# Kernel optimization log

Hardware: AMD Instinct MI355X
Metric: run time of the kernel (lower is better)

Reference implementation:

```python
import jax, jax.numpy as jnp
import numpy as np

N, E, IN_C, HID, OUT_C, HEADS, NUM_CLASSES = 50000, 800000, 128, 64, 64, 4, 40
NEG_SLOPE = 0.2


def _gat_conv(x, src, dst, W, a_src, a_dst, bias, heads, concat):
    # x: [N, F_in]; W: [F_in, heads*C]; a_src/a_dst: [1, heads, C]; bias: [out]
    n = x.shape[0]
    h = (x @ W).reshape(n, heads, -1)                      # [N, H, C]
    alpha_s = (h * a_src).sum(-1)                          # [N, H]
    alpha_d = (h * a_dst).sum(-1)                          # [N, H]
    e = jax.nn.leaky_relu(alpha_s[src] + alpha_d[dst], NEG_SLOPE)  # [E, H]
    # scatter-softmax over incoming edges of each dst node
    emax = jax.ops.segment_max(e, dst, num_segments=n)
    emax = jnp.where(jnp.isfinite(emax), emax, 0.0)
    ee = jnp.exp(e - emax[dst])
    denom = jax.ops.segment_sum(ee, dst, num_segments=n) + 1e-16
    w = ee / denom[dst]                                    # [E, H]
    out = jax.ops.segment_sum(h[src] * w[:, :, None], dst, num_segments=n)  # [N, H, C]
    out = out.reshape(n, -1) if concat else out.mean(axis=1)
    return out + bias


def setup_inputs() -> dict:
    key = jax.random.key(0)
    ks = jax.random.split(key, 12)
    s1 = 1.0 / np.sqrt(IN_C)
    s2 = 1.0 / np.sqrt(HID * HEADS)
    s3 = 1.0 / np.sqrt(OUT_C)
    return {
        "x": jax.random.normal(ks[0], (N, IN_C), dtype=jnp.float32),
        "edge_index": jax.random.randint(ks[1], (2, E), 0, N, dtype=jnp.int64),
        "W1": jax.random.normal(ks[2], (IN_C, HEADS * HID), dtype=jnp.float32) * s1,
        "att_src1": jax.random.normal(ks[3], (1, HEADS, HID), dtype=jnp.float32) * s1,
        "att_dst1": jax.random.normal(ks[4], (1, HEADS, HID), dtype=jnp.float32) * s1,
        "b1": jnp.zeros((HEADS * HID,), dtype=jnp.float32),
        "W2": jax.random.normal(ks[5], (HEADS * HID, OUT_C), dtype=jnp.float32) * s2,
        "att_src2": jax.random.normal(ks[6], (1, 1, OUT_C), dtype=jnp.float32) * s2,
        "att_dst2": jax.random.normal(ks[7], (1, 1, OUT_C), dtype=jnp.float32) * s2,
        "b2": jnp.zeros((OUT_C,), dtype=jnp.float32),
        "fc_w": jax.random.normal(ks[8], (OUT_C, NUM_CLASSES), dtype=jnp.float32) * s3,
        "fc_b": jnp.zeros((NUM_CLASSES,), dtype=jnp.float32),
    }


def reference(x, edge_index, W1, att_src1, att_dst1, b1, W2, att_src2, att_dst2, b2, fc_w, fc_b):
    n = x.shape[0]
    loops = jnp.arange(n, dtype=edge_index.dtype)
    ei = jnp.concatenate([edge_index, jnp.stack([loops, loops])], axis=1)  # add self-loops (PyG default)
    src, dst = ei[0], ei[1]
    h = jax.nn.relu(_gat_conv(x, src, dst, W1, att_src1, att_dst1, b1, HEADS, True))
    h = jax.nn.relu(_gat_conv(h, src, dst, W2, att_src2, att_dst2, b2, 1, False))
    # dropout p=0.01 is identity in eval mode
    pooled = h.mean(axis=0, keepdims=True)                 # global mean pool -> [1, OUT_C]
    logits = pooled @ fc_w + fc_b
    return jax.nn.log_softmax(logits, axis=1)
```

## Files before the change

### kernel.cpp

```cpp
#include <hip/hip_runtime.h>
#include <hip/hip_bf16.h>
#include <math.h>

#define NEG_SLOPE 0.2f
#define CHUNK2 2048
#define PGROUPS 32

typedef __attribute__((ext_vector_type(8))) short bf16x8;
typedef __attribute__((ext_vector_type(4))) float f32x4;
typedef __attribute__((ext_vector_type(2))) float f32x2_t;

__device__ __forceinline__ float lrelu(float a) { return a >= 0.f ? a : NEG_SLOPE * a; }
__device__ __forceinline__ unsigned short f2bu(float v) {
  unsigned u = __float_as_uint(v);
  u += 0x7fffu + ((u >> 16) & 1u);
  return (unsigned short)(u >> 16);
}
__device__ __forceinline__ unsigned char f2fp8(float v) {
  return (unsigned char)(__builtin_amdgcn_cvt_pk_fp8_f32(v, v, 0, false) & 0xFF);
}
__device__ __forceinline__ void fp8x4_dec(unsigned v, float& a, float& b, float& c, float& d) {
  f32x2_t lo = __builtin_amdgcn_cvt_pk_f32_fp8(v, false);
  f32x2_t hi = __builtin_amdgcn_cvt_pk_f32_fp8(v, true);
  a = lo.x; b = lo.y; c = hi.x; d = hi.y;
}

__global__ __launch_bounds__(256) void prep_kernel(
    const float* __restrict__ W1, unsigned short* __restrict__ w1t,
    const float* __restrict__ W2, unsigned short* __restrict__ w2t,
    const int* __restrict__ ei, int* __restrict__ bhist, int* __restrict__ done,
    int* __restrict__ bucketOff, int* __restrict__ cursor, int* __restrict__ rowptrN,
    float* __restrict__ pooled_grp,
    int E0, int Etot, int NBUCK, int wBlocks, int histBlocks) {
  __shared__ int hsm[256];
  __shared__ int rank;
  int t = threadIdx.x;
  if (blockIdx.x < (unsigned)wBlocks) {
    const int tot1 = 128 * 256, tot2 = 256 * 64;
    for (int i = blockIdx.x * 256 + t; i < tot1 + tot2; i += wBlocks * 256) {
      if (i < tot1) { int k = i >> 8, n = i & 255; w1t[n * 128 + k] = f2bu(W1[i]); }
      else { int j = i - tot1; int k = j >> 6, n = j & 63; w2t[n * 256 + k] = f2bu(W2[j]); }
    }
  } else {
    int bid = blockIdx.x - wBlocks;
    hsm[t] = 0;
    __syncthreads();
    for (int e = bid * 256 + t; e < Etot; e += histBlocks * 256) {
      int dst = (e < E0) ? ei[E0 + e] : (e - E0);
      atomicAdd(&hsm[dst >> 8], 1);
    }
    __syncthreads();
    if (t < NBUCK && hsm[t]) atomicAdd(&bhist[t], hsm[t]);
    __threadfence();
    if (t == 0) rank = atomicAdd(done, 1);
    __syncthreads();
    if (rank == histBlocks - 1) {
      int v = (t < NBUCK) ? atomicAdd(&bhist[t], 0) : 0;
      __syncthreads();
      hsm[t] = v;
      __syncthreads();
      for (int off = 1; off < 256; off <<= 1) {
        int u = (t >= off) ? hsm[t - off] : 0;
        __syncthreads();
        hsm[t] += u;
        __syncthreads();
      }
      int excl = hsm[t] - v;
      if (t < NBUCK) { bucketOff[t] = excl; cursor[t] = excl; }
      if (t == 0) { bucketOff[NBUCK] = Etot; *rowptrN = Etot; }
      for (int i = t; i < PGROUPS * 64; i += 256) pooled_grp[i] = 0.f;
    }
  }
}

__device__ void gemm1_tile(const float* __restrict__ x,
    const unsigned short* __restrict__ BT, unsigned char* __restrict__ C8,
    const float* __restrict__ att_s, const float* __restrict__ att_d,
    float* __restrict__ as_, float* __restrict__ ad_,
    int M, int bx, int by, char* smem) {
  const int K = 128;
  unsigned short (*Al)[40] = (unsigned short (*)[40])smem;
  unsigned short (*Bt)[40] = (unsigned short (*)[40])(smem + 5120);
  float* sal = (float*)(smem + 10240);
  float* sad = (float*)(smem + 10752);
  const int tid = threadIdx.x;
  const int row0 = by * 64, col0 = bx * 64;
  const int lane = tid & 63, wave = tid >> 6;
  const int wm = wave >> 1, wn = wave & 1;
  const int l15 = lane & 15, q = lane >> 4;

  f32x4 acc[2][2] = {};

  const int rr = tid >> 2, rc = (tid & 3) * 8;

  for (int k0 = 0; k0 < K; k0 += 32) {
    float4 v0 = make_float4(0.f, 0.f, 0.f, 0.f), v1 = v0;
    if (row0 + rr < M) {
      const float* ap = x + (size_t)(row0 + rr) * K + k0 + rc;
      v0 = *(const float4*)ap;
      v1 = *(const float4*)(ap + 4);
    }
    *(ushort4*)&Al[rr][rc] = make_ushort4(f2bu(v0.x), f2bu(v0.y), f2bu(v0.z), f2bu(v0.w));
    *(ushort4*)&Al[rr][rc + 4] = make_ushort4(f2bu(v1.x), f2bu(v1.y), f2bu(v1.z), f2bu(v1.w));
    {
      const ushort4* bp = (const ushort4*)(BT + (size_t)(col0 + rr) * K + k0 + rc);
      *(ushort4*)&Bt[rr][rc] = bp[0];
      *(ushort4*)&Bt[rr][rc + 4] = bp[1];
    }
    __syncthreads();
    bf16x8 af[2], bf[2];
#pragma unroll
    for (int mi = 0; mi < 2; mi++)
      af[mi] = *(const bf16x8*)&Al[wm * 32 + mi * 16 + l15][q * 8];
#pragma unroll
    for (int ni = 0; ni < 2; ni++)
      bf[ni] = *(const bf16x8*)&Bt[wn * 32 + ni * 16 + l15][q * 8];
#pragma unroll
    for (int mi = 0; mi < 2; mi++)
#pragma unroll
      for (int ni = 0; ni < 2; ni++)
        acc[mi][ni] = __builtin_amdgcn_mfma_f32_16x16x32_bf16(af[mi], bf[ni], acc[mi][ni], 0, 0, 0);
    __syncthreads();
  }
#pragma unroll
  for (int mi = 0; mi < 2; mi++) {
#pragma unroll
    for (int r = 0; r < 4; r++) {
      int grow = row0 + wm * 32 + mi * 16 + q * 4 + r;
      if (grow < M) {
#pragma unroll
        for (int ni = 0; ni < 2; ni++) {
          int gcol = col0 + wn * 32 + ni * 16 + l15;
          C8[(size_t)grow * 256 + gcol] = f2fp8(acc[mi][ni][r]);
        }
      }
    }
  }
  float atts0 = att_s[col0 + wn * 32 + l15];
  float atts1 = att_s[col0 + wn * 32 + 16 + l15];
  float attd0 = att_d[col0 + wn * 32 + l15];
  float attd1 = att_d[col0 + wn * 32 + 16 + l15];
#pragma unroll
  for (int mi = 0; mi < 2; mi++) {
#pragma unroll
    for (int r = 0; r < 4; r++) {
      float vs = acc[mi][0][r] * atts0 + acc[mi][1][r] * atts1;
      float vd = acc[mi][0][r] * attd0 + acc[mi][1][r] * attd1;
#pragma unroll
      for (int off = 1; off < 16; off <<= 1) {
        vs += __shfl_xor(vs, off);
        vd += __shfl_xor(vd, off);
      }
      if (l15 == 0) {
        int rl = wm * 32 + mi * 16 + q * 4 + r;
        sal[wn * 64 + rl] = vs;
        sad[wn * 64 + rl] = vd;
      }
    }
  }
  __syncthreads();
  if (tid < 64) {
    int grow = row0 + tid;
    if (grow < M) {
      as_[(size_t)grow * 4 + bx] = sal[tid] + sal[64 + tid];
      ad_[(size_t)grow * 4 + bx] = sad[tid] + sad[64 + tid];
    }
  }
}

__global__ __launch_bounds__(256) void gemm1_scatter_kernel(
    const float* __restrict__ x, const unsigned short* __restrict__ BT,
    unsigned char* __restrict__ C8, const float* __restrict__ att_s,
    const float* __restrict__ att_d, float* __restrict__ as_, float* __restrict__ ad_,
    int M, const int* __restrict__ ei, int* __restrict__ cursor, int* __restrict__ pairs,
    int E0, int Etot, int NBUCK, int NSC) {
  __shared__ __align__(16) char smem[18432];
  if (blockIdx.x < (unsigned)NSC) {
    int2* stage = (int2*)smem;
    int* h = (int*)(smem + 16384);
    int* base = (int*)(smem + 17408);
    int t = threadIdx.x;
    int e0 = blockIdx.x * CHUNK2;
    h[t] = 0;
    __syncthreads();
    int cnt = Etot - e0;
    if (cnt > CHUNK2) cnt = CHUNK2;
    for (int i = t; i < cnt; i += 256) {
      int e = e0 + i;
      int s, d;
      if (e < E0) { s = ei[e]; d = ei[E0 + e]; } else { s = d = e - E0; }
      stage[i] = make_int2((s << 8) | (d & 255), d >> 8);
      atomicAdd(&h[d >> 8], 1);
    }
    __syncthreads();
    if (t < NBUCK && h[t]) base[t] = atomicAdd(&cursor[t], h[t]);
    __syncthreads();
    for (int i = t; i < cnt; i += 256) {
      int2 p = stage[i];
      int pos = atomicAdd(&base[p.y], 1);
      pairs[pos] = p.x;
    }
  } else {
    int flat = blockIdx.x - NSC;
    gemm1_tile(x, BT, C8, att_s, att_d, as_, ad_, M, flat % 4, flat / 4, smem);
  }
}

__global__ __launch_bounds__(256) void csr_build_kernel(const int* __restrict__ pairs,
    const int* __restrict__ bucketOff, int* __restrict__ rowptr, int* __restrict__ csr_src,
    int N) {
  int b = blockIdx.x, t = threadIdx.x;
  int base = bucketOff[b], cnt = bucketOff[b + 1] - base;
  int n0 = b << 8;
  __shared__ int h[256];
  __shared__ int s[256];
  __shared__ int ex[256];
  h[t] = 0;
  __syncthreads();
  for (int i = t; i < cnt; i += 256) atomicAdd(&h[pairs[base + i] & 255], 1);
  __syncthreads();
  int v = h[t];
  s[t] = v;
  __syncthreads();
  for (int off = 1; off < 256; off <<= 1) {
    int u = (t >= off) ? s[t - off] : 0;
    __syncthreads();
    s[t] += u;
    __syncthreads();
  }
  ex[t] = s[t] - v;
  if (n0 + t < N) rowptr[n0 + t] = base + ex[t];
  __syncthreads();
  for (int i = t; i < cnt; i += 256) {
    int p = pairs[base + i];
    int pos = atomicAdd(&ex[p & 255], 1);
    csr_src[base + pos] = ((unsigned)p) >> 8;
  }
}

#define ACC16(W, X) do {                                                       \
    float c0_, c1_, c2_, c3_;                                                  \
    fp8x4_dec((X).x, c0_, c1_, c2_, c3_);                                      \
    acc[0] = fmaf((W), c0_, acc[0]);  acc[1] = fmaf((W), c1_, acc[1]);         \
    acc[2] = fmaf((W), c2_, acc[2]);  acc[3] = fmaf((W), c3_, acc[3]);         \
    fp8x4_dec((X).y, c0_, c1_, c2_, c3_);                                      \
    acc[4] = fmaf((W), c0_, acc[4]);  acc[5] = fmaf((W), c1_, acc[5]);         \
    acc[6] = fmaf((W), c2_, acc[6]);  acc[7] = fmaf((W), c3_, acc[7]);         \
    fp8x4_dec((X).z, c0_, c1_, c2_, c3_);                                      \
    acc[8] = fmaf((W), c0_, acc[8]);  acc[9] = fmaf((W), c1_, acc[9]);         \
    acc[10] = fmaf((W), c2_, acc[10]); acc[11] = fmaf((W), c3_, acc[11]);      \
    fp8x4_dec((X).w, c0_, c1_, c2_, c3_);                                      \
    acc[12] = fmaf((W), c0_, acc[12]); acc[13] = fmaf((W), c1_, acc[13]);      \
    acc[14] = fmaf((W), c2_, acc[14]); acc[15] = fmaf((W), c3_, acc[15]);      \
  } while (0)

__global__ __launch_bounds__(256) void aggr1_gemm2_kernel(const int* __restrict__ rowptr,
    const int* __restrict__ csr_src, const float* __restrict__ as_,
    const float* __restrict__ ad_, const uint4* __restrict__ h1f8,
    const float* __restrict__ b1, const unsigned short* __restrict__ w2t,
    const float* __restrict__ att_s2, const float* __restrict__ att_d2,
    unsigned char* __restrict__ h2, float* __restrict__ as2, float* __restrict__ ad2,
    int Nn) {
  __shared__ __align__(16) char As[16 * 512];
  __shared__ float sal[64], sad[64];
  int lane = threadIdx.x & 63, wv = threadIdx.x >> 6;
  int q = lane >> 4, l15 = lane & 15;
  int nloc = wv * 4 + q;
  int base = blockIdx.x * 16;
  int n = base + nloc;
  bool active = n < Nn;
  int row = 0, deg = 0;
  if (active) { row = rowptr[n], deg = rowptr[n + 1] - row; }
  int rowEnd = row + deg;
  int hh = l15 >> 2;
  float adv = active ? ad_[n * 4 + hh] : 0.f;
  const uint4* hb = h1f8 + l15;
  float acc[16] = {};
  float wsum = 0.f;
  int p0 = row + l15;
  int idxv = (p0 < rowEnd) ? csr_src[p0] : 0;
  for (int s0 = 0; s0 < deg; s0 += 16) {
    int pn = row + s0 + 16 + l15;
    int idxn = (pn < rowEnd) ? csr_src[pn] : 0;
    int m = deg - s0;
    if (m > 16) m = 16;
    int j = 0;
    for (; j + 4 <= m; j += 4) {
      int i0 = __shfl(idxv, j, 16);
      int i1 = __shfl(idxv, j + 1, 16);
      int i2 = __shfl(idxv, j + 2, 16);
      int i3 = __shfl(idxv, j + 3, 16);
      float a0v = as_[i0 * 4 + hh];
      float a1v = as_[i1 * 4 + hh];
      float a2v = as_[i2 * 4 + hh];
      float a3v = as_[i3 * 4 + hh];
      uint4 x0 = hb[(size_t)i0 * 16];
      uint4 x1 = hb[(size_t)i1 * 16];
      uint4 x2 = hb[(size_t)i2 * 16];
      uint4 x3 = hb[(size_t)i3 * 16];
      float w0 = __expf(lrelu(a0v + adv));
      float w1 = __expf(lrelu(a1v + adv));
      float w2 = __expf(lrelu(a2v + adv));
      float w3 = __expf(lrelu(a3v + adv));
      wsum += (w0 + w1) + (w2 + w3);
      ACC16(w0, x0);
      ACC16(w1, x1);
      ACC16(w2, x2);
      ACC16(w3, x3);
    }
    for (; j < m; j++) {
      int i0 = __shfl(idxv, j, 16);
      float a0v = as_[i0 * 4 + hh];
      uint4 x0 = hb[(size_t)i0 * 16];
      float w0 = __expf(lrelu(a0v + adv));
      wsum += w0;
      ACC16(w0, x0);
    }
    idxv = idxn;
  }
  float vinv = (deg > 0) ? 1.f / wsum : 0.f;
  int c0i = l15 * 16;
  unsigned short ob[16];
#pragma unroll
  for (int k = 0; k < 4; k++) {
    float4 bb = *(const float4*)(b1 + c0i + k * 4);
    float r0 = fmaf(acc[k * 4 + 0], vinv, bb.x);
    float r1 = fmaf(acc[k * 4 + 1], vinv, bb.y);
    float r2 = fmaf(acc[k * 4 + 2], vinv, bb.z);
    float r3 = fmaf(acc[k * 4 + 3], vinv, bb.w);
    ob[k * 4 + 0] = f2bu(r0 > 0.f ? r0 : 0.f);
    ob[k * 4 + 1] = f2bu(r1 > 0.f ? r1 : 0.f);
    ob[k * 4 + 2] = f2bu(r2 > 0.f ? r2 : 0.f);
    ob[k * 4 + 3] = f2bu(r3 > 0.f ? r3 : 0.f);
  }
#pragma unroll
  for (int j = 0; j < 4; j++)
    *(ushort4*)(As + nloc * 512 + ((l15 * 32 + j * 8) ^ ((nloc & 7) << 4))) =
        *(ushort4*)&ob[j * 4];
  __syncthreads();

  bf16x8 bfr[8];
#pragma unroll
  for (int k = 0; k < 8; k++)
    bfr[k] = *(const bf16x8*)(w2t + (size_t)(wv * 16 + l15) * 256 + k * 32 + q * 8);
  f32x4 acc2 = {};
#pragma unroll
  for (int k = 0; k < 8; k++) {
    bf16x8 af = *(const bf16x8*)(As + l15 * 512 + ((k * 64 + q * 16) ^ ((l15 & 7) << 4)));
    acc2 = __builtin_amdgcn_mfma_f32_16x16x32_bf16(af, bfr[k], acc2, 0, 0, 0);
  }
  float atts = att_s2[wv * 16 + l15], attd = att_d2[wv * 16 + l15];
#pragma unroll
  for (int r = 0; r < 4; r++) {
    int node = q * 4 + r;
    int grow = base + node;
    if (grow < Nn) h2[(size_t)grow * 64 + wv * 16 + l15] = f2fp8(acc2[r]);
    float vs = acc2[r] * atts;
    float vd = acc2[r] * attd;
#pragma unroll
    for (int off = 1; off < 16; off <<= 1) {
      vs += __shfl_xor(vs, off);
      vd += __shfl_xor(vd, off);
    }
    if (l15 == 0) {
      sal[wv * 16 + node] = vs;
      sad[wv * 16 + node] = vd;
    }
  }
  __syncthreads();
  if (threadIdx.x < 16 && base + (int)threadIdx.x < Nn) {
    int t = threadIdx.x;
    as2[base + t] = sal[t] + sal[16 + t] + sal[32 + t] + sal[48 + t];
    ad2[base + t] = sad[t] + sad[16 + t] + sad[32 + t] + sad[48 + t];
  }
}

__global__ __launch_bounds__(256) void aggr2_pool_kernel(const int* __restrict__ rowptr,
    const int* __restrict__ csr_src, const float* __restrict__ as_,
    const float* __restrict__ ad_, const unsigned* __restrict__ h2f8,
    const float* __restrict__ b2, float* __restrict__ pooled_grp, int Nn) {
  int lane = threadIdx.x & 63, wv = threadIdx.x >> 6;
  int q = lane >> 4, l15 = lane & 15;
  int c0 = l15 * 4;
  const unsigned* hb = h2f8 + l15;
  float p0 = 0.f, p1 = 0.f, p2 = 0.f, p3 = 0.f;
  int stream = (blockIdx.x * 4 + wv) * 4 + q;
  int nstreams = gridDim.x * 16;
  for (int n = stream; n < Nn; n += nstreams) {
    int row = rowptr[n], deg = rowptr[n + 1] - row;
    int rowEnd = row + deg;
    float adv = ad_[n];
    float a0 = 0.f, a1 = 0.f, a2 = 0.f, a3 = 0.f, wsum = 0.f;
    int pp = row + l15;
    int idxv = (pp < rowEnd) ? csr_src[pp] : 0;
    for (int s0 = 0; s0 < deg; s0 += 16) {
      int pn = row + s0 + 16 + l15;
      int idxn = (pn < rowEnd) ? csr_src[pn] : 0;
      int m = deg - s0;
      if (m > 16) m = 16;
      int j = 0;
      for (; j + 8 <= m; j += 8) {
        int id[8];
        float al[8];
        unsigned xv[8];
#pragma unroll
        for (int u = 0; u < 8; u++) id[u] = __shfl(idxv, j + u, 16);
#pragma unroll
        for (int u = 0; u < 8; u++) al[u] = as_[id[u]];
#pragma unroll
        for (int u = 0; u < 8; u++) xv[u] = hb[(size_t)id[u] * 16];
#pragma unroll
        for (int u = 0; u < 8; u++) {
          float w = __expf(lrelu(al[u] + adv));
          wsum += w;
          float c0f, c1f, c2f, c3f;
          fp8x4_dec(xv[u], c0f, c1f, c2f, c3f);
          a0 = fmaf(w, c0f, a0); a1 = fmaf(w, c1f, a1);
          a2 = fmaf(w, c2f, a2); a3 = fmaf(w, c3f, a3);
        }
      }
      for (; j + 4 <= m; j += 4) {
        int id[4];
        float al[4];
        unsigned xv[4];
#pragma unroll
        for (int u = 0; u < 4; u++) id[u] = __shfl(idxv, j + u, 16);
#pragma unroll
        for (int u = 0; u < 4; u++) al[u] = as_[id[u]];
#pragma unroll
        for (int u = 0; u < 4; u++) xv[u] = hb[(size_t)id[u] * 16];
#pragma unroll
        for (int u = 0; u < 4; u++) {
          float w = __expf(lrelu(al[u] + adv));
          wsum += w;
          float c0f, c1f, c2f, c3f;
          fp8x4_dec(xv[u], c0f, c1f, c2f, c3f);
          a0 = fmaf(w, c0f, a0); a1 = fmaf(w, c1f, a1);
          a2 = fmaf(w, c2f, a2); a3 = fmaf(w, c3f, a3);
        }
      }
      for (; j < m; j++) {
        int i0 = __shfl(idxv, j, 16);
        float w = __expf(lrelu(as_[i0] + adv));
        wsum += w;
        float c0f, c1f, c2f, c3f;
        fp8x4_dec(hb[(size_t)i0 * 16], c0f, c1f, c2f, c3f);
        a0 = fmaf(w, c0f, a0); a1 = fmaf(w, c1f, a1);
        a2 = fmaf(w, c2f, a2); a3 = fmaf(w, c3f, a3);
      }
      idxv = idxn;
    }
    float vinv = 1.f / wsum;
    float4 bb = *(const float4*)(b2 + c0);
    float r0 = fmaf(a0, vinv, bb.x), r1 = fmaf(a1, vinv, bb.y);
    float r2 = fmaf(a2, vinv, bb.z), r3 = fmaf(a3, vinv, bb.w);
    p0 += r0 > 0.f ? r0 : 0.f; p1 += r1 > 0.f ? r1 : 0.f;
    p2 += r2 > 0.f ? r2 : 0.f; p3 += r3 > 0.f ? r3 : 0.f;
  }
  __shared__ float4 sred[4][4][16];
  sred[wv][q][l15] = make_float4(p0, p1, p2, p3);
  __syncthreads();
  if (threadIdx.x < 64) {
    int slot = threadIdx.x >> 2, comp = threadIdx.x & 3;
    float acc = 0.f;
#pragma unroll
    for (int i = 0; i < 4; i++)
#pragma unroll
      for (int j = 0; j < 4; j++) {
        float4 v = sred[i][j][slot];
        acc += comp == 0 ? v.x : (comp == 1 ? v.y : (comp == 2 ? v.z : v.w));
      }
    atomicAdd(&pooled_grp[(blockIdx.x & (PGROUPS - 1)) * 64 + slot * 4 + comp], acc);
  }
}

__global__ __launch_bounds__(64) void pool_head_kernel(const float* __restrict__ pooled_grp,
    const float* __restrict__ fc_w, const float* __restrict__ fc_b,
    float* __restrict__ out, float invN) {
  int t = threadIdx.x;
  __shared__ float pl[64];
  __shared__ float lg[40];
  __shared__ float lse;
  float acc = 0.f;
#pragma unroll
  for (int g = 0; g < PGROUPS; g++) acc += pooled_grp[g * 64 + t];
  pl[t] = acc * invN;
  __syncthreads();
  if (t < 40) {
    float sm = fc_b[t];
    for (int c = 0; c < 64; c++) sm = fmaf(pl[c], fc_w[c * 40 + t], sm);
    lg[t] = sm;
  }
  __syncthreads();
  if (t == 0) {
    float m = -1e30f;
    for (int j = 0; j < 40; j++) m = fmaxf(m, lg[j]);
    float su = 0.f;
    for (int j = 0; j < 40; j++) su += expf(lg[j] - m);
    lse = m + logf(su);
  }
  __syncthreads();
  if (t < 40) out[t] = lg[t] - lse;
}

extern "C" void kernel_launch(void* const* d_in, const int* in_sizes, int n_in,
                              void* d_out, int out_size, void* d_ws, size_t ws_size,
                              hipStream_t stream) {
  const float* x        = (const float*)d_in[0];
  const int*   ei       = (const int*)d_in[1];
  const float* W1       = (const float*)d_in[2];
  const float* att_src1 = (const float*)d_in[3];
  const float* att_dst1 = (const float*)d_in[4];
  const float* b1       = (const float*)d_in[5];
  const float* W2       = (const float*)d_in[6];
  const float* att_src2 = (const float*)d_in[7];
  const float* att_dst2 = (const float*)d_in[8];
  const float* b2       = (const float*)d_in[9];
  const float* fc_w     = (const float*)d_in[10];
  const float* fc_b     = (const float*)d_in[11];
  float* out = (float*)d_out;

  const int N    = in_sizes[0] / 128;
  const int E0   = in_sizes[1] / 2;
  const int Etot = E0 + N;
  const int NBUCK = (N + 255) >> 8;
  const int NSC  = (Etot + CHUNK2 - 1) / CHUNK2;
  const int GBY  = (N + 63) / 64;
  const int AGG2_BLOCKS = 2048;

  char* wsb = (char*)d_ws;
  size_t o = 0;
  auto alloc = [&](size_t bytes) { char* p = wsb + o; o += (bytes + 15) & ~(size_t)15; return p; };
  unsigned short* w1t  = (unsigned short*)alloc(256 * 128 * 2);
  unsigned short* w2t  = (unsigned short*)alloc(64 * 256 * 2);
  unsigned char*  h1f8 = (unsigned char*)alloc((size_t)N * 256);
  unsigned char*  h2   = (unsigned char*)alloc((size_t)N * 64);
  float* as1  = (float*)alloc((size_t)N * 4 * 4);
  float* ad1  = (float*)alloc((size_t)N * 4 * 4);
  float* as2  = (float*)alloc((size_t)N * 4);
  float* ad2  = (float*)alloc((size_t)N * 4);
  int* rowptr = (int*)alloc((size_t)(N + 1) * 4);
  int* bhist  = (int*)alloc(260 * 4);
  int* bucketOff = (int*)alloc(257 * 4);
  int* cursor = (int*)alloc(256 * 4);
  int* pairs  = (int*)alloc((size_t)Etot * 4);
  int* csr_src = (int*)alloc((size_t)Etot * 4);
  float* pooled_grp = (float*)alloc((size_t)PGROUPS * 64 * 4);
  int* done = bhist + 256;

  dim3 blk(256);

  hipMemsetAsync(bhist, 0, 257 * sizeof(int), stream);
  prep_kernel<<<16 + 256, blk, 0, stream>>>(
      W1, w1t, W2, w2t, ei, bhist, done, bucketOff, cursor, rowptr + N, pooled_grp,
      E0, Etot, NBUCK, 16, 256);

  gemm1_scatter_kernel<<<NSC + 4 * GBY, blk, 0, stream>>>(
      x, w1t, h1f8, att_src1, att_dst1, as1, ad1, N,
      ei, cursor, pairs, E0, Etot, NBUCK, NSC);
  csr_build_kernel<<<NBUCK, blk, 0, stream>>>(pairs, bucketOff, rowptr, csr_src, N);

  aggr1_gemm2_kernel<<<(N + 15) / 16, blk, 0, stream>>>(
      rowptr, csr_src, as1, ad1, (const uint4*)h1f8, b1, w2t, att_src2, att_dst2,
      h2, as2, ad2, N);

  aggr2_pool_kernel<<<AGG2_BLOCKS, blk, 0, stream>>>(rowptr, csr_src, as2, ad2,
                                                     (const unsigned*)h2, b2, pooled_grp, N);

  pool_head_kernel<<<1, 64, 0, stream>>>(pooled_grp, fc_w, fc_b, out, 1.0f / (float)N);
}
```

Before: 243.2 us.

## Sort nodes by degree for balanced aggregation and use packed fp8 decode FMAs

Measured after the change: 549.2 us. 126% more time.

```diff
diff --git a/kernel.cpp b/kernel.cpp
--- a/kernel.cpp
+++ b/kernel.cpp
@@ -208,13 +208,14 @@
 
 __global__ __launch_bounds__(256) void csr_build_kernel(const int* __restrict__ pairs,
     const int* __restrict__ bucketOff, int* __restrict__ rowptr, int* __restrict__ csr_src,
-    int N) {
+    int* __restrict__ dhist, int* __restrict__ done2, int* __restrict__ dcur, int N) {
   int b = blockIdx.x, t = threadIdx.x;
   int base = bucketOff[b], cnt = bucketOff[b + 1] - base;
   int n0 = b << 8;
   __shared__ int h[256];
   __shared__ int s[256];
   __shared__ int ex[256];
+  __shared__ int rank2;
   h[t] = 0;
   __syncthreads();
   for (int i = t; i < cnt; i += 256) atomicAdd(&h[pairs[base + i] & 255], 1);
@@ -229,29 +230,56 @@
     __syncthreads();
   }
   ex[t] = s[t] - v;
-  if (n0 + t < N) rowptr[n0 + t] = base + ex[t];
+  if (n0 + t < N) {
+    rowptr[n0 + t] = base + ex[t];
+    int bin = (v > 255) ? 0 : (255 - v);
+    atomicAdd(&dhist[bin], 1);
+  }
   __syncthreads();
   for (int i = t; i < cnt; i += 256) {
     int p = pairs[base + i];
     int pos = atomicAdd(&ex[p & 255], 1);
     csr_src[base + pos] = ((unsigned)p) >> 8;
   }
-}
-
-#define ACC16(W, X) do {                                                       \
-    float c0_, c1_, c2_, c3_;                                                  \
-    fp8x4_dec((X).x, c0_, c1_, c2_, c3_);                                      \
-    acc[0] = fmaf((W), c0_, acc[0]);  acc[1] = fmaf((W), c1_, acc[1]);         \
-    acc[2] = fmaf((W), c2_, acc[2]);  acc[3] = fmaf((W), c3_, acc[3]);         \
-    fp8x4_dec((X).y, c0_, c1_, c2_, c3_);                                      \
-    acc[4] = fmaf((W), c0_, acc[4]);  acc[5] = fmaf((W), c1_, acc[5]);         \
-    acc[6] = fmaf((W), c2_, acc[6]);  acc[7] = fmaf((W), c3_, acc[7]);         \
-    fp8x4_dec((X).z, c0_, c1_, c2_, c3_);                                      \
-    acc[8] = fmaf((W), c0_, acc[8]);  acc[9] = fmaf((W), c1_, acc[9]);         \
-    acc[10] = fmaf((W), c2_, acc[10]); acc[11] = fmaf((W), c3_, acc[11]);      \
-    fp8x4_dec((X).w, c0_, c1_, c2_, c3_);                                      \
-    acc[12] = fmaf((W), c0_, acc[12]); acc[13] = fmaf((W), c1_, acc[13]);      \
-    acc[14] = fmaf((W), c2_, acc[14]); acc[15] = fmaf((W), c3_, acc[15]);      \
+  __threadfence();
+  if (t == 0) rank2 = atomicAdd(done2, 1);
+  __syncthreads();
+  if (rank2 == gridDim.x - 1) {
+    int hv = atomicAdd(&dhist[t], 0);
+    __syncthreads();
+    s[t] = hv;
+    __syncthreads();
+    for (int off = 1; off < 256; off <<= 1) {
+      int u = (t >= off) ? s[t - off] : 0;
+      __syncthreads();
+      s[t] += u;
+      __syncthreads();
+    }
+    dcur[t] = s[t] - hv;
+  }
+}
+
+__global__ __launch_bounds__(256) void place_kernel(const int* __restrict__ rowptr,
+    int* __restrict__ dcur, int* __restrict__ perm, int N) {
+  int n = blockIdx.x * 256 + threadIdx.x;
+  if (n < N) {
+    int deg = rowptr[n + 1] - rowptr[n];
+    int bin = (deg > 255) ? 0 : (255 - deg);
+    int pos = atomicAdd(&dcur[bin], 1);
+    perm[pos] = n;
+  }
+}
+
+#define ACCV(W, X) do {                                                        \
+    f32x2_t w2_; w2_.x = (W); w2_.y = (W);                                     \
+    av[0] += w2_ * __builtin_amdgcn_cvt_pk_f32_fp8((X).x, false);              \
+    av[1] += w2_ * __builtin_amdgcn_cvt_pk_f32_fp8((X).x, true);               \
+    av[2] += w2_ * __builtin_amdgcn_cvt_pk_f32_fp8((X).y, false);              \
+    av[3] += w2_ * __builtin_amdgcn_cvt_pk_f32_fp8((X).y, true);               \
+    av[4] += w2_ * __builtin_amdgcn_cvt_pk_f32_fp8((X).z, false);              \
+    av[5] += w2_ * __builtin_amdgcn_cvt_pk_f32_fp8((X).z, true);               \
+    av[6] += w2_ * __builtin_amdgcn_cvt_pk_f32_fp8((X).w, false);              \
+    av[7] += w2_ * __builtin_amdgcn_cvt_pk_f32_fp8((X).w, true);               \
   } while (0)
 
 __global__ __launch_bounds__(256) void aggr1_gemm2_kernel(const int* __restrict__ rowptr,
@@ -259,23 +287,26 @@
     const float* __restrict__ ad_, const uint4* __restrict__ h1f8,
     const float* __restrict__ b1, const unsigned short* __restrict__ w2t,
     const float* __restrict__ att_s2, const float* __restrict__ att_d2,
+    const int* __restrict__ perm,
     unsigned char* __restrict__ h2, float* __restrict__ as2, float* __restrict__ ad2,
     int Nn) {
   __shared__ __align__(16) char As[16 * 512];
   __shared__ float sal[64], sad[64];
+  __shared__ int snode[16];
   int lane = threadIdx.x & 63, wv = threadIdx.x >> 6;
   int q = lane >> 4, l15 = lane & 15;
   int nloc = wv * 4 + q;
   int base = blockIdx.x * 16;
-  int n = base + nloc;
-  bool active = n < Nn;
+  bool active = (base + nloc) < Nn;
+  int n = active ? perm[base + nloc] : -1;
+  if (l15 == 0) snode[nloc] = n;
   int row = 0, deg = 0;
   if (active) { row = rowptr[n], deg = rowptr[n + 1] - row; }
   int rowEnd = row + deg;
   int hh = l15 >> 2;
   float adv = active ? ad_[n * 4 + hh] : 0.f;
   const uint4* hb = h1f8 + l15;
-  float acc[16] = {};
+  f32x2_t av[8] = {};
   float wsum = 0.f;
   int p0 = row + l15;
   int idxv = (p0 < rowEnd) ? csr_src[p0] : 0;
@@ -303,10 +334,10 @@
       float w2 = __expf(lrelu(a2v + adv));
       float w3 = __expf(lrelu(a3v + adv));
       wsum += (w0 + w1) + (w2 + w3);
-      ACC16(w0, x0);
-      ACC16(w1, x1);
-      ACC16(w2, x2);
-      ACC16(w3, x3);
+      ACCV(w0, x0);
+      ACCV(w1, x1);
+      ACCV(w2, x2);
+      ACCV(w3, x3);
     }
     for (; j < m; j++) {
       int i0 = __shfl(idxv, j, 16);
@@ -314,7 +345,7 @@
       uint4 x0 = hb[(size_t)i0 * 16];
       float w0 = __expf(lrelu(a0v + adv));
       wsum += w0;
-      ACC16(w0, x0);
+      ACCV(w0, x0);
     }
     idxv = idxn;
   }
@@ -324,10 +355,10 @@
 #pragma unroll
   for (int k = 0; k < 4; k++) {
     float4 bb = *(const float4*)(b1 + c0i + k * 4);
-    float r0 = fmaf(acc[k * 4 + 0], vinv, bb.x);
-    float r1 = fmaf(acc[k * 4 + 1], vinv, bb.y);
-    float r2 = fmaf(acc[k * 4 + 2], vinv, bb.z);
-    float r3 = fmaf(acc[k * 4 + 3], vinv, bb.w);
+    float r0 = fmaf(av[k * 2].x, vinv, bb.x);
+    float r1 = fmaf(av[k * 2].y, vinv, bb.y);
+    float r2 = fmaf(av[k * 2 + 1].x, vinv, bb.z);
+    float r3 = fmaf(av[k * 2 + 1].y, vinv, bb.w);
     ob[k * 4 + 0] = f2bu(r0 > 0.f ? r0 : 0.f);
     ob[k * 4 + 1] = f2bu(r1 > 0.f ? r1 : 0.f);
     ob[k * 4 + 2] = f2bu(r2 > 0.f ? r2 : 0.f);
@@ -353,8 +384,8 @@
 #pragma unroll
   for (int r = 0; r < 4; r++) {
     int node = q * 4 + r;
-    int grow = base + node;
-    if (grow < Nn) h2[(size_t)grow * 64 + wv * 16 + l15] = f2fp8(acc2[r]);
+    int sn = snode[node];
+    if (sn >= 0) h2[(size_t)sn * 64 + wv * 16 + l15] = f2fp8(acc2[r]);
     float vs = acc2[r] * atts;
     float vd = acc2[r] * attd;
 #pragma unroll
@@ -368,29 +399,35 @@
     }
   }
   __syncthreads();
-  if (threadIdx.x < 16 && base + (int)threadIdx.x < Nn) {
+  if (threadIdx.x < 16) {
     int t = threadIdx.x;
-    as2[base + t] = sal[t] + sal[16 + t] + sal[32 + t] + sal[48 + t];
-    ad2[base + t] = sad[t] + sad[16 + t] + sad[32 + t] + sad[48 + t];
+    int sn = snode[t];
+    if (sn >= 0) {
+      as2[sn] = sal[t] + sal[16 + t] + sal[32 + t] + sal[48 + t];
+      ad2[sn] = sad[t] + sad[16 + t] + sad[32 + t] + sad[48 + t];
+    }
   }
 }
 
 __global__ __launch_bounds__(256) void aggr2_pool_kernel(const int* __restrict__ rowptr,
     const int* __restrict__ csr_src, const float* __restrict__ as_,
     const float* __restrict__ ad_, const unsigned* __restrict__ h2f8,
-    const float* __restrict__ b2, float* __restrict__ pooled_grp, int Nn) {
+    const float* __restrict__ b2, const int* __restrict__ perm,
+    float* __restrict__ pooled_grp, int Nn) {
   int lane = threadIdx.x & 63, wv = threadIdx.x >> 6;
   int q = lane >> 4, l15 = lane & 15;
   int c0 = l15 * 4;
   const unsigned* hb = h2f8 + l15;
-  float p0 = 0.f, p1 = 0.f, p2 = 0.f, p3 = 0.f;
+  f32x2_t pv0 = {0.f, 0.f}, pv1 = {0.f, 0.f};
   int stream = (blockIdx.x * 4 + wv) * 4 + q;
   int nstreams = gridDim.x * 16;
-  for (int n = stream; n < Nn; n += nstreams) {
+  for (int nn = stream; nn < Nn; nn += nstreams) {
+    int n = perm[nn];
     int row = rowptr[n], deg = rowptr[n + 1] - row;
     int rowEnd = row + deg;
     float adv = ad_[n];
-    float a0 = 0.f, a1 = 0.f, a2 = 0.f, a3 = 0.f, wsum = 0.f;
+    f32x2_t a01 = {0.f, 0.f}, a23 = {0.f, 0.f};
+    float wsum = 0.f;
     int pp = row + l15;
     int idxv = (pp < rowEnd) ? csr_src[pp] : 0;
     for (int s0 = 0; s0 < deg; s0 += 16) {
@@ -413,10 +450,9 @@
         for (int u = 0; u < 8; u++) {
           float w = __expf(lrelu(al[u] + adv));
           wsum += w;
-          float c0f, c1f, c2f, c3f;
-          fp8x4_dec(xv[u], c0f, c1f, c2f, c3f);
-          a0 = fmaf(w, c0f, a0); a1 = fmaf(w, c1f, a1);
-          a2 = fmaf(w, c2f, a2); a3 = fmaf(w, c3f, a3);
+          f32x2_t w2_; w2_.x = w; w2_.y = w;
+          a01 += w2_ * __builtin_amdgcn_cvt_pk_f32_fp8(xv[u], false);
+          a23 += w2_ * __builtin_amdgcn_cvt_pk_f32_fp8(xv[u], true);
         }
       }
       for (; j + 4 <= m; j += 4) {
@@ -433,32 +469,31 @@
         for (int u = 0; u < 4; u++) {
           float w = __expf(lrelu(al[u] + adv));
           wsum += w;
-          float c0f, c1f, c2f, c3f;
-          fp8x4_dec(xv[u], c0f, c1f, c2f, c3f);
-          a0 = fmaf(w, c0f, a0); a1 = fmaf(w, c1f, a1);
-          a2 = fmaf(w, c2f, a2); a3 = fmaf(w, c3f, a3);
+          f32x2_t w2_; w2_.x = w; w2_.y = w;
+          a01 += w2_ * __builtin_amdgcn_cvt_pk_f32_fp8(xv[u], false);
+          a23 += w2_ * __builtin_amdgcn_cvt_pk_f32_fp8(xv[u], true);
         }
       }
       for (; j < m; j++) {
         int i0 = __shfl(idxv, j, 16);
         float w = __expf(lrelu(as_[i0] + adv));
         wsum += w;
-        float c0f, c1f, c2f, c3f;
-        fp8x4_dec(hb[(size_t)i0 * 16], c0f, c1f, c2f, c3f);
-        a0 = fmaf(w, c0f, a0); a1 = fmaf(w, c1f, a1);
-        a2 = fmaf(w, c2f, a2); a3 = fmaf(w, c3f, a3);
+        unsigned xvv = hb[(size_t)i0 * 16];
+        f32x2_t w2_; w2_.x = w; w2_.y = w;
+        a01 += w2_ * __builtin_amdgcn_cvt_pk_f32_fp8(xvv, false);
+        a23 += w2_ * __builtin_amdgcn_cvt_pk_f32_fp8(xvv, true);
       }
       idxv = idxn;
     }
     float vinv = 1.f / wsum;
     float4 bb = *(const float4*)(b2 + c0);
-    float r0 = fmaf(a0, vinv, bb.x), r1 = fmaf(a1, vinv, bb.y);
-    float r2 = fmaf(a2, vinv, bb.z), r3 = fmaf(a3, vinv, bb.w);
-    p0 += r0 > 0.f ? r0 : 0.f; p1 += r1 > 0.f ? r1 : 0.f;
-    p2 += r2 > 0.f ? r2 : 0.f; p3 += r3 > 0.f ? r3 : 0.f;
+    float r0 = fmaf(a01.x, vinv, bb.x), r1 = fmaf(a01.y, vinv, bb.y);
+    float r2 = fmaf(a23.x, vinv, bb.z), r3 = fmaf(a23.y, vinv, bb.w);
+    pv0.x += r0 > 0.f ? r0 : 0.f; pv0.y += r1 > 0.f ? r1 : 0.f;
+    pv1.x += r2 > 0.f ? r2 : 0.f; pv1.y += r3 > 0.f ? r3 : 0.f;
   }
   __shared__ float4 sred[4][4][16];
-  sred[wv][q][l15] = make_float4(p0, p1, p2, p3);
+  sred[wv][q][l15] = make_float4(pv0.x, pv0.y, pv1.x, pv1.y);
   __syncthreads();
   if (threadIdx.x < 64) {
     int slot = threadIdx.x >> 2, comp = threadIdx.x & 3;
@@ -540,17 +575,22 @@
   float* as2  = (float*)alloc((size_t)N * 4);
   float* ad2  = (float*)alloc((size_t)N * 4);
   int* rowptr = (int*)alloc((size_t)(N + 1) * 4);
-  int* bhist  = (int*)alloc(260 * 4);
+  int* ctrl   = (int*)alloc(514 * 4);
   int* bucketOff = (int*)alloc(257 * 4);
   int* cursor = (int*)alloc(256 * 4);
+  int* dcur   = (int*)alloc(256 * 4);
+  int* perm   = (int*)alloc((size_t)N * 4);
   int* pairs  = (int*)alloc((size_t)Etot * 4);
   int* csr_src = (int*)alloc((size_t)Etot * 4);
   float* pooled_grp = (float*)alloc((size_t)PGROUPS * 64 * 4);
-  int* done = bhist + 256;
+  int* bhist = ctrl;
+  int* done  = ctrl + 256;
+  int* dhist = ctrl + 257;
+  int* done2 = ctrl + 513;
 
   dim3 blk(256);
 
-  hipMemsetAsync(bhist, 0, 257 * sizeof(int), stream);
+  hipMemsetAsync(ctrl, 0, 514 * sizeof(int), stream);
   prep_kernel<<<16 + 256, blk, 0, stream>>>(
       W1, w1t, W2, w2t, ei, bhist, done, bucketOff, cursor, rowptr + N, pooled_grp,
       E0, Etot, NBUCK, 16, 256);
@@ -558,14 +598,17 @@
   gemm1_scatter_kernel<<<NSC + 4 * GBY, blk, 0, stream>>>(
       x, w1t, h1f8, att_src1, att_dst1, as1, ad1, N,
       ei, cursor, pairs, E0, Etot, NBUCK, NSC);
-  csr_build_kernel<<<NBUCK, blk, 0, stream>>>(pairs, bucketOff, rowptr, csr_src, N);
+  csr_build_kernel<<<NBUCK, blk, 0, stream>>>(pairs, bucketOff, rowptr, csr_src,
+                                              dhist, done2, dcur, N);
+  place_kernel<<<(N + 255) / 256, blk, 0, stream>>>(rowptr, dcur, perm, N);
 
   aggr1_gemm2_kernel<<<(N + 15) / 16, blk, 0, stream>>>(
       rowptr, csr_src, as1, ad1, (const uint4*)h1f8, b1, w2t, att_src2, att_dst2,
-      h2, as2, ad2, N);
+      perm, h2, as2, ad2, N);
 
   aggr2_pool_kernel<<<AGG2_BLOCKS, blk, 0, stream>>>(rowptr, csr_src, as2, ad2,
-                                                     (const unsigned*)h2, b2, pooled_grp, N);
+                                                     (const unsigned*)h2, b2, perm,
+                                                     pooled_grp, N);
 
   pool_head_kernel<<<1, 64, 0, stream>>>(pooled_grp, fc_w, fc_b, out, 1.0f / (float)N);
 }
```
